# Performance work log

Hardware: AMD Instinct MI355X
Metric: run time of the kernel (lower is better)

## Reference

```python
import jax, jax.numpy as jnp
import numpy as np

LN_EPS = 1e-5
NEG_SLOPE = 0.01

def layer_norm(h, gamma, beta):
    mu = jnp.mean(h, axis=-1, keepdims=True)
    var = jnp.var(h, axis=-1, keepdims=True)
    return (h - mu) * jax.lax.rsqrt(var + LN_EPS) * gamma + beta

def setup_inputs() -> dict:
    key = jax.random.key(0)
    ks = jax.random.split(key, 12)
    N, E = 50000, 600000
    D_NODE, D_EDGE, D_IN = 128, 64, 192  # D_IN = D_NODE + D_EDGE
    x = jax.random.normal(ks[0], (N, D_NODE), dtype=jnp.float32)
    edge_index = jax.random.randint(ks[1], (2, E), 0, N, dtype=jnp.int64)
    edge_attr = jax.random.normal(ks[2], (E, D_EDGE), dtype=jnp.float32)
    # mlp_before_agg: Linear(192->128) + LayerNorm + LeakyReLU
    W1 = jax.random.normal(ks[3], (D_IN, D_NODE), dtype=jnp.float32) / np.sqrt(D_IN)
    b1 = jnp.zeros((D_NODE,), dtype=jnp.float32)
    g1 = jnp.ones((D_NODE,), dtype=jnp.float32)
    be1 = jnp.zeros((D_NODE,), dtype=jnp.float32)
    # mlp_after_agg: Linear(128->128) + LayerNorm + LeakyReLU
    W2 = jax.random.normal(ks[4], (D_NODE, D_NODE), dtype=jnp.float32) / np.sqrt(D_NODE)
    b2 = jnp.zeros((D_NODE,), dtype=jnp.float32)
    g2 = jnp.ones((D_NODE,), dtype=jnp.float32)
    be2 = jnp.zeros((D_NODE,), dtype=jnp.float32)
    return {"x": x, "edge_index": edge_index, "edge_attr": edge_attr,
            "W1": W1, "b1": b1, "g1": g1, "be1": be1,
            "W2": W2, "b2": b2, "g2": g2, "be2": be2}

def reference(x, edge_index, edge_attr, W1, b1, g1, be1, W2, b2, g2, be2):
    N = x.shape[0]
    row, col = edge_index[0], edge_index[1]
    # 1. gather + concat: (E, D_NODE + D_EDGE)
    out = jnp.concatenate([x[row], edge_attr], axis=1)
    # 2. pre-agg MLP: Linear + LayerNorm + LeakyReLU
    out = jax.nn.leaky_relu(layer_norm(out @ W1 + b1, g1, be1), NEG_SLOPE)
    # 3. scatter-mean aggregate over destination nodes (empty segments -> 0)
    sums = jax.ops.segment_sum(out, col, num_segments=N)
    counts = jax.ops.segment_sum(jnp.ones((out.shape[0], 1), out.dtype), col, num_segments=N)
    out = sums / jnp.maximum(counts, 1.0)
    # 4. post-agg MLP + residual + activation
    out = jax.nn.leaky_relu(layer_norm(out @ W2 + b2, g2, be2), NEG_SLOPE)
    return jax.nn.leaky_relu(out + x, NEG_SLOPE)
```

## Files before the change

kernel.cpp:

```cpp
#include <hip/hip_runtime.h>

#define D_NODE 128
#define D_EDGE 64
#define D_IN   192
#define NEG    0.01f
#define LN_EPS 1e-5f

typedef short bf16x8 __attribute__((ext_vector_type(8)));
typedef float f32x4  __attribute__((ext_vector_type(4)));

__device__ __forceinline__ unsigned f2bf(float f) {
    unsigned u = __builtin_bit_cast(unsigned, f);
    return (u + 0x7FFFu + ((u >> 16) & 1u)) >> 16;
}
__device__ __forceinline__ unsigned pk2(float a, float b) {
    return f2bf(a) | (f2bf(b) << 16);
}
__device__ __forceinline__ float bf2f(unsigned short s) {
    unsigned u = ((unsigned)s) << 16;
    return __builtin_bit_cast(float, u);
}

__global__ void k_hist(const int* __restrict__ ei, int* __restrict__ hist, int E) {
    int i = blockIdx.x * blockDim.x + threadIdx.x;
    int stride = gridDim.x * blockDim.x;
    for (int e = i; e < E; e += stride) atomicAdd(&hist[ei[E + e]], 1);
}

__global__ __launch_bounds__(1024) void k_scanA(const int* __restrict__ hist,
                                                int* __restrict__ base,
                                                int* __restrict__ blockTot, int N) {
    __shared__ int wsum[16], woff[16];
    const int t = threadIdx.x, b = blockIdx.x;
    const int i = b * 1024 + t;
    const int lane = t & 63, w = t >> 6;
    int v = (i < N) ? hist[i] : 0;
    int x = v;
    #pragma unroll
    for (int d = 1; d < 64; d <<= 1) { int u = __shfl_up(x, d); if (lane >= d) x += u; }
    if (lane == 63) wsum[w] = x;
    __syncthreads();
    if (t < 16) {
        int y = wsum[t];
        #pragma unroll
        for (int d = 1; d < 16; d <<= 1) { int u = __shfl_up(y, d, 16); if (t >= d) y += u; }
        woff[t] = y - wsum[t];
    }
    __syncthreads();
    int incl = x + woff[w];
    if (i < N) base[i] = incl - v;
    if (t == 1023) blockTot[b] = incl;
}

__global__ void k_scanB(int* __restrict__ blockTot, int NB) {
    int t = threadIdx.x;
    int v = (t < NB) ? blockTot[t] : 0;
    int x = v;
    #pragma unroll
    for (int d = 1; d < 64; d <<= 1) { int u = __shfl_up(x, d); if (t >= d) x += u; }
    if (t < NB) blockTot[t] = x - v;
}

__global__ __launch_bounds__(1024) void k_scanC(int* __restrict__ base,
                                                const int* __restrict__ blockTot, int N) {
    int i = blockIdx.x * 1024 + threadIdx.x;
    if (i < N) base[i] += blockTot[blockIdx.x];
}

__global__ void k_bucket(const int* __restrict__ ei, int* __restrict__ base,
                         int* __restrict__ perm, int* __restrict__ srcrow,
                         int* __restrict__ dstcol, int E) {
    int i = blockIdx.x * blockDim.x + threadIdx.x;
    int stride = gridDim.x * blockDim.x;
    for (int e = i; e < E; e += stride) {
        int c = ei[E + e];
        int r = ei[e];
        int p = atomicAdd(&base[c], 1);
        perm[p]   = e;
        srcrow[p] = r;
        dstcol[p] = c;
    }
}

__global__ __launch_bounds__(256) void edge_mfma_seg(
    const float* __restrict__ x,
    const float* __restrict__ edge_attr,
    const int*   __restrict__ perm,
    const int*   __restrict__ srcrow,
    const int*   __restrict__ dstcol,
    const float* __restrict__ W1,
    const float* __restrict__ b1,
    const float* __restrict__ g1,
    const float* __restrict__ be1,
    float* __restrict__ sums,
    int E, int ntiles)
{
    __shared__ unsigned short h[64][200];
    __shared__ float rS [64][4], rS2[64][4];
    __shared__ int   scol[64];
    __shared__ unsigned long long maskSh;

    const int tid = threadIdx.x;
    const int w   = tid >> 6;
    const int l   = tid & 63;
    const int lm  = l & 15;
    const int q   = l >> 4;
    const int q8  = q * 8;

    bf16x8 Bfr[2][6];
    float  b1v[2], g1v[2], bev[2];
    #pragma unroll
    for (int c2 = 0; c2 < 2; ++c2) {
        const int n = (2 * w + c2) * 16 + lm;
        b1v[c2] = b1[n]; g1v[c2] = g1[n]; bev[c2] = be1[n];
        #pragma unroll
        for (int kt = 0; kt < 6; ++kt) {
            bf16x8 f;
            #pragma unroll
            for (int j = 0; j < 8; ++j)
                f[j] = (short)f2bf(W1[(kt * 32 + q8 + j) * 128 + n]);
            Bfr[c2][kt] = f;
        }
    }

    for (int tile = blockIdx.x; tile < ntiles; tile += gridDim.x) {
        const int e0 = tile * 64;

        {
            const int e  = tid >> 2;
            const int qq = tid & 3;
            const int ge = e0 + e;
            if (ge < E) {
                const int row = srcrow[ge];
                const int eid = perm[ge];
                const float4* xr = (const float4*)(x + (size_t)row * D_NODE);
                #pragma unroll
                for (int i = 0; i < 8; ++i) {
                    float4 v = xr[qq * 8 + i];
                    *(uint2*)&h[e][qq * 32 + i * 4] =
                        make_uint2(pk2(v.x, v.y), pk2(v.z, v.w));
                }
                const float4* ar = (const float4*)(edge_attr + (size_t)eid * D_EDGE);
                #pragma unroll
                for (int i = 0; i < 4; ++i) {
                    float4 v = ar[qq * 4 + i];
                    *(uint2*)&h[e][128 + qq * 16 + i * 4] =
                        make_uint2(pk2(v.x, v.y), pk2(v.z, v.w));
                }
            } else {
                #pragma unroll
                for (int i = 0; i < 8; ++i)
                    *(uint2*)&h[e][qq * 32 + i * 4] = make_uint2(0u, 0u);
                #pragma unroll
                for (int i = 0; i < 4; ++i)
                    *(uint2*)&h[e][128 + qq * 16 + i * 4] = make_uint2(0u, 0u);
            }
            if (tid < 64)
                scol[tid] = (e0 + tid < E) ? dstcol[e0 + tid] : -1;
        }
        __syncthreads();

        f32x4 acc[4][2];
        #pragma unroll
        for (int et = 0; et < 4; ++et)
            #pragma unroll
            for (int c2 = 0; c2 < 2; ++c2)
                acc[et][c2] = (f32x4){0.f, 0.f, 0.f, 0.f};

        #pragma unroll
        for (int et = 0; et < 4; ++et) {
            bf16x8 Afr[6];
            #pragma unroll
            for (int kt = 0; kt < 6; ++kt)
                Afr[kt] = *(const bf16x8*)&h[et * 16 + lm][kt * 32 + q8];
            #pragma unroll
            for (int c2 = 0; c2 < 2; ++c2)
                #pragma unroll
                for (int kt = 0; kt < 6; ++kt)
                    acc[et][c2] = __builtin_amdgcn_mfma_f32_16x16x32_bf16(
                        Afr[kt], Bfr[c2][kt], acc[et][c2], 0, 0, 0);
        }

        #pragma unroll
        for (int et = 0; et < 4; ++et) {
            #pragma unroll
            for (int r = 0; r < 4; ++r) {
                float v0 = acc[et][0][r] + b1v[0];
                float v1 = acc[et][1][r] + b1v[1];
                acc[et][0][r] = v0;
                acc[et][1][r] = v1;
                float s  = v0 + v1;
                float s2 = v0 * v0 + v1 * v1;
                #pragma unroll
                for (int off = 1; off < 16; off <<= 1) {
                    s  += __shfl_xor(s,  off, 16);
                    s2 += __shfl_xor(s2, off, 16);
                }
                if (lm == 0) {
                    const int em = et * 16 + q * 4 + r;
                    rS [em][w] = s;
                    rS2[em][w] = s2;
                }
            }
        }
        __syncthreads();

        if (tid < 64) {
            int me = scol[tid];
            int pv = (tid == 0) ? (me ^ 1) : scol[tid - 1];
            unsigned long long m = __ballot(me != pv);
            if (tid == 0) maskSh = m;
        }

        #pragma unroll
        for (int et = 0; et < 4; ++et) {
            #pragma unroll
            for (int r = 0; r < 4; ++r) {
                const int em = et * 16 + q * 4 + r;
                float4 p  = *(const float4*)&rS [em][0];
                float4 p2 = *(const float4*)&rS2[em][0];
                const float S    = (p.x  + p.y)  + (p.z  + p.w);
                const float S2   = (p2.x + p2.y) + (p2.z + p2.w);
                const float mu   = S * (1.f / 128.f);
                const float var  = S2 * (1.f / 128.f) - mu * mu;
                const float rstd = rsqrtf(var + LN_EPS);
                #pragma unroll
                for (int c2 = 0; c2 < 2; ++c2) {
                    float y = (acc[et][c2][r] - mu) * rstd * g1v[c2] + bev[c2];
                    y = (y > 0.f) ? y : NEG * y;
                    h[em][(2 * w + c2) * 16 + lm] = (unsigned short)f2bf(y);
                }
            }
        }
        __syncthreads();

        {
            const unsigned long long mask = maskSh;
            const int g  = tid >> 7;
            const int j  = tid & 127;
            const int lo = g * 32, hi = lo + 32;
            float s = 0.f;
            int rs = lo;
            for (int em = lo; em < hi; ++em) {
                s += bf2f(h[em][j]);
                const int nx = em + 1;
                const bool isEnd = (nx == hi) || ((mask >> nx) & 1ull);
                if (isEnd) {
                    const int dest = scol[em];
                    if (dest >= 0) {
                        const bool sg = (rs > 0) && ((mask >> rs) & 1ull);
                        const bool eg = (em < 63) && ((mask >> nx) & 1ull);
                        float* p = &sums[(size_t)dest * D_NODE + j];
                        if (sg && eg) *p = s;
                        else          atomicAdd(p, s);
                    }
                    s = 0.f; rs = nx;
                }
            }
        }
        __syncthreads();
    }
}

__global__ __launch_bounds__(256) void node_mfma(
    const float* __restrict__ sums,
    const int*   __restrict__ hist,
    const float* __restrict__ x,
    const float* __restrict__ W2,
    const float* __restrict__ b2,
    const float* __restrict__ g2,
    const float* __restrict__ be2,
    float* __restrict__ out,
    int N)
{
    __shared__ unsigned short h[64][136];
    __shared__ float rS [64][4], rS2[64][4];

    const int tid = threadIdx.x;
    const int w   = tid >> 6;
    const int l   = tid & 63;
    const int lm  = l & 15;
    const int q   = l >> 4;
    const int q8  = q * 8;

    bf16x8 Bfr[2][4];
    float  b2v[2], g2v[2], bev[2];
    #pragma unroll
    for (int c2 = 0; c2 < 2; ++c2) {
        const int n = (2 * w + c2) * 16 + lm;
        b2v[c2] = b2[n]; g2v[c2] = g2[n]; bev[c2] = be2[n];
        #pragma unroll
        for (int kt = 0; kt < 4; ++kt) {
            bf16x8 f;
            #pragma unroll
            for (int j = 0; j < 8; ++j)
                f[j] = (short)f2bf(W2[(kt * 32 + q8 + j) * 128 + n]);
            Bfr[c2][kt] = f;
        }
    }

    const int n0 = blockIdx.x * 64;

    {
        const int e  = tid >> 2;
        const int qq = tid & 3;
        const int gn = n0 + e;
        if (gn < N) {
            const int cnt = hist[gn];
            const float sc = (cnt > 0) ? 1.f / (float)cnt : 0.f;
            const float4* sr = (const float4*)(sums + (size_t)gn * D_NODE);
            #pragma unroll
            for (int i = 0; i < 8; ++i) {
                float4 v = sr[qq * 8 + i];
                *(uint2*)&h[e][qq * 32 + i * 4] =
                    make_uint2(pk2(v.x * sc, v.y * sc), pk2(v.z * sc, v.w * sc));
            }
        } else {
            #pragma unroll
            for (int i = 0; i < 8; ++i)
                *(uint2*)&h[e][qq * 32 + i * 4] = make_uint2(0u, 0u);
        }
    }
    __syncthreads();

    f32x4 acc[4][2];
    #pragma unroll
    for (int et = 0; et < 4; ++et)
        #pragma unroll
        for (int c2 = 0; c2 < 2; ++c2)
            acc[et][c2] = (f32x4){0.f, 0.f, 0.f, 0.f};

    #pragma unroll
    for (int et = 0; et < 4; ++et) {
        bf16x8 Afr[4];
        #pragma unroll
        for (int kt = 0; kt < 4; ++kt)
            Afr[kt] = *(const bf16x8*)&h[et * 16 + lm][kt * 32 + q8];
        #pragma unroll
        for (int c2 = 0; c2 < 2; ++c2)
            #pragma unroll
            for (int kt = 0; kt < 4; ++kt)
                acc[et][c2] = __builtin_amdgcn_mfma_f32_16x16x32_bf16(
                    Afr[kt], Bfr[c2][kt], acc[et][c2], 0, 0, 0);
    }

    #pragma unroll
    for (int et = 0; et < 4; ++et) {
        #pragma unroll
        for (int r = 0; r < 4; ++r) {
            float v0 = acc[et][0][r] + b2v[0];
            float v1 = acc[et][1][r] + b2v[1];
            acc[et][0][r] = v0;
            acc[et][1][r] = v1;
            float s  = v0 + v1;
            float s2 = v0 * v0 + v1 * v1;
            #pragma unroll
            for (int off = 1; off < 16; off <<= 1) {
                s  += __shfl_xor(s,  off, 16);
                s2 += __shfl_xor(s2, off, 16);
            }
            if (lm == 0) {
                const int em = et * 16 + q * 4 + r;
                rS [em][w] = s;
                rS2[em][w] = s2;
            }
        }
    }
    __syncthreads();

    #pragma unroll
    for (int et = 0; et < 4; ++et) {
        #pragma unroll
        for (int r = 0; r < 4; ++r) {
            const int em = et * 16 + q * 4 + r;
            const int gn = n0 + em;
            if (gn >= N) continue;
            float4 p  = *(const float4*)&rS [em][0];
            float4 p2 = *(const float4*)&rS2[em][0];
            const float S    = (p.x  + p.y)  + (p.z  + p.w);
            const float S2   = (p2.x + p2.y) + (p2.z + p2.w);
            const float mu   = S * (1.f / 128.f);
            const float var  = S2 * (1.f / 128.f) - mu * mu;
            const float rstd = rsqrtf(var + LN_EPS);
            #pragma unroll
            for (int c2 = 0; c2 < 2; ++c2) {
                const int col = (2 * w + c2) * 16 + lm;
                float y = (acc[et][c2][r] - mu) * rstd * g2v[c2] + bev[c2];
                y = (y > 0.f) ? y : NEG * y;
                float rr = y + x[(size_t)gn * D_NODE + col];
                rr = (rr > 0.f) ? rr : NEG * rr;
                out[(size_t)gn * D_NODE + col] = rr;
            }
        }
    }
}

extern "C" void kernel_launch(void* const* d_in, const int* in_sizes, int n_in,
                              void* d_out, int out_size, void* d_ws, size_t ws_size,
                              hipStream_t stream) {
    const float* x          = (const float*)d_in[0];
    const int*   edge_index = (const int*)  d_in[1];
    const float* edge_attr  = (const float*)d_in[2];
    const float* W1         = (const float*)d_in[3];
    const float* b1         = (const float*)d_in[4];
    const float* g1         = (const float*)d_in[5];
    const float* be1        = (const float*)d_in[6];
    const float* W2         = (const float*)d_in[7];
    const float* b2         = (const float*)d_in[8];
    const float* g2         = (const float*)d_in[9];
    const float* be2        = (const float*)d_in[10];

    const int N = in_sizes[0] / D_NODE;
    const int E = in_sizes[1] / 2;

    float* sums     = (float*)d_ws;
    int*   hist     = (int*)(sums + (size_t)N * D_NODE);
    int*   base     = hist + N;
    int*   blockTot = base + N;
    int*   perm     = blockTot + 64;
    int*   srcrow   = perm + E;
    int*   dstcol   = srcrow + E;

    hipMemsetAsync(d_ws, 0, ((size_t)N * D_NODE + (size_t)N) * sizeof(float), stream);

    k_hist<<<dim3(256), dim3(256), 0, stream>>>(edge_index, hist, E);
    const int NB = (N + 1023) / 1024;
    k_scanA<<<dim3(NB), dim3(1024), 0, stream>>>(hist, base, blockTot, N);
    k_scanB<<<dim3(1),  dim3(64),   0, stream>>>(blockTot, NB);
    k_scanC<<<dim3(NB), dim3(1024), 0, stream>>>(base, blockTot, N);
    k_bucket<<<dim3(256), dim3(256), 0, stream>>>(edge_index, base, perm, srcrow, dstcol, E);

    const int ntiles = (E + 63) / 64;
    const int grid   = ntiles < 1280 ? ntiles : 1280;
    edge_mfma_seg<<<dim3(grid), dim3(256), 0, stream>>>(
        x, edge_attr, perm, srcrow, dstcol, W1, b1, g1, be1, sums, E, ntiles);

    node_mfma<<<dim3((N + 63) / 64), dim3(256), 0, stream>>>(
        sums, hist, x, W2, b2, g2, be2, (float*)d_out, N);
}
```

Measured before the change: 510.1 us.

## Pre-pack x to bf16 and do segment reduction via MFMA with run-indicator matrix

Adds a kernel that converts x to bf16 once, so the edge kernel gathers half the bytes with 16-byte copies instead of converting per edge. The serial per-column segment-sum scan is replaced by an MFMA product of the transposed activations with a one-hot run-membership matrix, both held in swizzled LDS. Interior runs are written with plain vector stores and the boundary runs of each tile use atomics. It also sets a launch-bounds occupancy hint of 5 blocks per SM. The cost is an extra pass over x, extra LDS traffic and MFMA work sized to the number of runs per tile.

```diff
diff --git a/kernel.cpp b/kernel.cpp
--- a/kernel.cpp
+++ b/kernel.cpp
@@ -16,9 +16,19 @@
 __device__ __forceinline__ unsigned pk2(float a, float b) {
     return f2bf(a) | (f2bf(b) << 16);
 }
-__device__ __forceinline__ float bf2f(unsigned short s) {
-    unsigned u = ((unsigned)s) << 16;
-    return __builtin_bit_cast(float, u);
+
+__global__ void k_packx(const float* __restrict__ x, unsigned short* __restrict__ xb,
+                        int n8) {
+    int i = blockIdx.x * blockDim.x + threadIdx.x;
+    int stride = gridDim.x * blockDim.x;
+    for (int t = i; t < n8; t += stride) {
+        const float4* p = (const float4*)x + (size_t)t * 2;
+        float4 a = p[0], b = p[1];
+        uint4 o;
+        o.x = pk2(a.x, a.y); o.y = pk2(a.z, a.w);
+        o.z = pk2(b.x, b.y); o.w = pk2(b.z, b.w);
+        ((uint4*)xb)[t] = o;
+    }
 }
 
 __global__ void k_hist(const int* __restrict__ ei, int* __restrict__ hist, int E) {
@@ -82,8 +92,8 @@
     }
 }
 
-__global__ __launch_bounds__(256) void edge_mfma_seg(
-    const float* __restrict__ x,
+__global__ __launch_bounds__(256, 5) void edge_mfma_seg(
+    const unsigned short* __restrict__ xb,
     const float* __restrict__ edge_attr,
     const int*   __restrict__ perm,
     const int*   __restrict__ srcrow,
@@ -95,10 +105,14 @@
     float* __restrict__ sums,
     int E, int ntiles)
 {
-    __shared__ unsigned short h[64][200];
+    __shared__ __align__(16) unsigned short h[64][200];
     __shared__ float rS [64][4], rS2[64][4];
     __shared__ int   scol[64];
-    __shared__ unsigned long long maskSh;
+    __shared__ int   rdest[64];
+    __shared__ int   nruns_sh;
+
+    unsigned short (*yT)[64] = (unsigned short (*)[64])(&h[0][0]);
+    unsigned short (*PT)[64] = (unsigned short (*)[64])((char*)(&h[0][0]) + 16384);
 
     const int tid = threadIdx.x;
     const int w   = tid >> 6;
@@ -133,27 +147,28 @@
             if (ge < E) {
                 const int row = srcrow[ge];
                 const int eid = perm[ge];
-                const float4* xr = (const float4*)(x + (size_t)row * D_NODE);
-                #pragma unroll
-                for (int i = 0; i < 8; ++i) {
-                    float4 v = xr[qq * 8 + i];
-                    *(uint2*)&h[e][qq * 32 + i * 4] =
-                        make_uint2(pk2(v.x, v.y), pk2(v.z, v.w));
-                }
+                const uint4* xr = (const uint4*)(xb + (size_t)row * D_NODE);
+                #pragma unroll
+                for (int i = 0; i < 4; ++i)
+                    *(uint4*)&h[e][qq * 32 + i * 8] = xr[qq * 4 + i];
                 const float4* ar = (const float4*)(edge_attr + (size_t)eid * D_EDGE);
                 #pragma unroll
-                for (int i = 0; i < 4; ++i) {
-                    float4 v = ar[qq * 4 + i];
-                    *(uint2*)&h[e][128 + qq * 16 + i * 4] =
-                        make_uint2(pk2(v.x, v.y), pk2(v.z, v.w));
+                for (int i = 0; i < 2; ++i) {
+                    float4 v0 = ar[qq * 4 + 2 * i];
+                    float4 v1 = ar[qq * 4 + 2 * i + 1];
+                    uint4 o;
+                    o.x = pk2(v0.x, v0.y); o.y = pk2(v0.z, v0.w);
+                    o.z = pk2(v1.x, v1.y); o.w = pk2(v1.z, v1.w);
+                    *(uint4*)&h[e][128 + qq * 16 + i * 8] = o;
                 }
             } else {
-                #pragma unroll
-                for (int i = 0; i < 8; ++i)
-                    *(uint2*)&h[e][qq * 32 + i * 4] = make_uint2(0u, 0u);
+                uint4 z = make_uint4(0u, 0u, 0u, 0u);
                 #pragma unroll
                 for (int i = 0; i < 4; ++i)
-                    *(uint2*)&h[e][128 + qq * 16 + i * 4] = make_uint2(0u, 0u);
+                    *(uint4*)&h[e][qq * 32 + i * 8] = z;
+                #pragma unroll
+                for (int i = 0; i < 2; ++i)
+                    *(uint4*)&h[e][128 + qq * 16 + i * 8] = z;
             }
             if (tid < 64)
                 scol[tid] = (e0 + tid < E) ? dstcol[e0 + tid] : -1;
@@ -206,14 +221,23 @@
         __syncthreads();
 
         if (tid < 64) {
+            uint4 z = make_uint4(0u, 0u, 0u, 0u);
+            #pragma unroll
+            for (int i = 0; i < 8; ++i)
+                *(uint4*)&PT[tid][i * 8] = z;
             int me = scol[tid];
             int pv = (tid == 0) ? (me ^ 1) : scol[tid - 1];
             unsigned long long m = __ballot(me != pv);
-            if (tid == 0) maskSh = m;
+            int run = __popcll(m & ((2ull << tid) - 1)) - 1;
+            if (me != pv) rdest[run] = me;
+            if (tid == 0) nruns_sh = (int)__popcll(m);
+            int ep = (tid & 7) | ((((tid >> 3) ^ (run & 7)) & 7) << 3);
+            PT[run][ep] = 0x3F80;
         }
 
         #pragma unroll
         for (int et = 0; et < 4; ++et) {
+            float yv[2][4];
             #pragma unroll
             for (int r = 0; r < 4; ++r) {
                 const int em = et * 16 + q * 4 + r;
@@ -228,33 +252,67 @@
                 for (int c2 = 0; c2 < 2; ++c2) {
                     float y = (acc[et][c2][r] - mu) * rstd * g1v[c2] + bev[c2];
                     y = (y > 0.f) ? y : NEG * y;
-                    h[em][(2 * w + c2) * 16 + lm] = (unsigned short)f2bf(y);
-                }
+                    yv[c2][r] = y;
+                }
+            }
+            #pragma unroll
+            for (int c2 = 0; c2 < 2; ++c2) {
+                const int col = (2 * w + c2) * 16 + lm;
+                const int em0 = et * 16 + q * 4;
+                const int ch  = ((em0 >> 3) ^ (col & 7)) & 7;
+                uint2 o;
+                o.x = pk2(yv[c2][0], yv[c2][1]);
+                o.y = pk2(yv[c2][2], yv[c2][3]);
+                *(uint2*)&yT[col][ch * 8 + (q & 1) * 4] = o;
             }
         }
         __syncthreads();
 
         {
-            const unsigned long long mask = maskSh;
-            const int g  = tid >> 7;
-            const int j  = tid & 127;
-            const int lo = g * 32, hi = lo + 32;
-            float s = 0.f;
-            int rs = lo;
-            for (int em = lo; em < hi; ++em) {
-                s += bf2f(h[em][j]);
-                const int nx = em + 1;
-                const bool isEnd = (nx == hi) || ((mask >> nx) & 1ull);
-                if (isEnd) {
-                    const int dest = scol[em];
+            bf16x8 afr[2][2];
+            #pragma unroll
+            for (int ct = 0; ct < 2; ++ct)
+                #pragma unroll
+                for (int kt = 0; kt < 2; ++kt) {
+                    const int col = w * 32 + ct * 16 + lm;
+                    const int ch  = ((kt * 4 + q) ^ (col & 7)) & 7;
+                    afr[ct][kt] = *(const bf16x8*)&yT[col][ch * 8];
+                }
+            const int nr = nruns_sh;
+            for (int rt = 0; rt * 16 < nr; ++rt) {
+                bf16x8 bfr[2];
+                #pragma unroll
+                for (int kt = 0; kt < 2; ++kt) {
+                    const int rr = rt * 16 + lm;
+                    const int ch = ((kt * 4 + q) ^ (rr & 7)) & 7;
+                    bfr[kt] = *(const bf16x8*)&PT[rr][ch * 8];
+                }
+                f32x4 o0 = (f32x4){0.f, 0.f, 0.f, 0.f};
+                f32x4 o1 = (f32x4){0.f, 0.f, 0.f, 0.f};
+                #pragma unroll
+                for (int kt = 0; kt < 2; ++kt) {
+                    o0 = __builtin_amdgcn_mfma_f32_16x16x32_bf16(
+                        afr[0][kt], bfr[kt], o0, 0, 0, 0);
+                    o1 = __builtin_amdgcn_mfma_f32_16x16x32_bf16(
+                        afr[1][kt], bfr[kt], o1, 0, 0, 0);
+                }
+                const int run = rt * 16 + lm;
+                if (run < nr) {
+                    const int dest = rdest[run];
                     if (dest >= 0) {
-                        const bool sg = (rs > 0) && ((mask >> rs) & 1ull);
-                        const bool eg = (em < 63) && ((mask >> nx) & 1ull);
-                        float* p = &sums[(size_t)dest * D_NODE + j];
-                        if (sg && eg) *p = s;
-                        else          atomicAdd(p, s);
+                        const bool at = (run == 0) || (run == nr - 1);
+                        float* p0 = &sums[(size_t)dest * D_NODE + w * 32 + q * 4];
+                        if (at) {
+                            #pragma unroll
+                            for (int r = 0; r < 4; ++r) {
+                                atomicAdd(&p0[r],      o0[r]);
+                                atomicAdd(&p0[16 + r], o1[r]);
+                            }
+                        } else {
+                            *(f32x4*)p0        = o0;
+                            *(f32x4*)(p0 + 16) = o1;
+                        }
                     }
-                    s = 0.f; rs = nx;
                 }
             }
         }
@@ -273,7 +331,7 @@
     float* __restrict__ out,
     int N)
 {
-    __shared__ unsigned short h[64][136];
+    __shared__ __align__(16) unsigned short h[64][136];
     __shared__ float rS [64][4], rS2[64][4];
 
     const int tid = threadIdx.x;
@@ -420,8 +478,12 @@
     int*   perm     = blockTot + 64;
     int*   srcrow   = perm + E;
     int*   dstcol   = srcrow + E;
+    unsigned short* xb = (unsigned short*)(dstcol + E);
 
     hipMemsetAsync(d_ws, 0, ((size_t)N * D_NODE + (size_t)N) * sizeof(float), stream);
+
+    const int n8 = N * (D_NODE / 8);
+    k_packx<<<dim3(1024), dim3(256), 0, stream>>>(x, xb, n8);
 
     k_hist<<<dim3(256), dim3(256), 0, stream>>>(edge_index, hist, E);
     const int NB = (N + 1023) / 1024;
@@ -433,7 +495,7 @@
     const int ntiles = (E + 63) / 64;
     const int grid   = ntiles < 1280 ? ntiles : 1280;
     edge_mfma_seg<<<dim3(grid), dim3(256), 0, stream>>>(
-        x, edge_attr, perm, srcrow, dstcol, W1, b1, g1, be1, sums, E, ntiles);
+        xb, edge_attr, perm, srcrow, dstcol, W1, b1, g1, be1, sums, E, ntiles);
 
     node_mfma<<<dim3((N + 63) / 64), dim3(256), 0, stream>>>(
         sums, hist, x, W2, b2, g2, be2, (float*)d_out, N);
```

Measured after the change: 566.5 us. 11.0% more time.
